# Kernel tuning notes

Measured on AMD Instinct MI355X. Metric: run time of the kernel, lower is better.

The kernel has to match this reference:

```python
import jax, jax.numpy as jnp
import numpy as np

B, S, D, H = 16, 1024, 512, 8
DH = D // H


def setup_inputs() -> dict:
    key = jax.random.key(0)
    ks = jax.random.split(key, 8)
    q = jax.random.normal(ks[0], (B, S, D), dtype=jnp.float32)
    k = jax.random.normal(ks[1], (B, S, D), dtype=jnp.float32)
    v = jax.random.normal(ks[2], (B, S, D), dtype=jnp.float32)
    # causal lower-triangular mask (1 = attend), broadcastable [1,1,S,S]
    mask = jnp.tril(jnp.ones((S, S), dtype=jnp.int32))[None, None]
    # xavier-uniform weights, zero biases (matches _reset_parameters)
    def xavier(rk, fan):
        lim = float(np.sqrt(6.0 / (fan + fan)))
        return jax.random.uniform(rk, (fan, fan), jnp.float32, -lim, lim)
    Wk = xavier(ks[3], D)
    Wv = xavier(ks[4], D)
    Wo = xavier(ks[5], D)
    bk = jnp.zeros((D,), jnp.float32)
    bv = jnp.zeros((D,), jnp.float32)
    bo = jnp.zeros((D,), jnp.float32)
    return {"q": q, "k": k, "v": v, "mask": mask,
            "Wk": Wk, "bk": bk, "Wv": Wv, "bv": bv, "Wo": Wo, "bo": bo,
            "zero_pad": 1}


def reference(q, k, v, mask, Wk, bk, Wv, bv, Wo, bo, zero_pad):
    # key_query_same=True: q and k both use key_linear
    def split_heads(x):  # [B,S,D] -> [B,H,S,DH]
        return x.reshape(B, S, H, DH).transpose(0, 2, 1, 3)

    qh = split_heads(q @ Wk.T + bk)
    kh = split_heads(k @ Wk.T + bk)
    vh = split_heads(v @ Wv.T + bv)

    scores = jnp.einsum('bhqd,bhkd->bhqk', qh, kh) / jnp.sqrt(jnp.float32(DH))
    scores = jnp.where(mask == 0, jnp.float32(-1e32), scores)
    attn = jax.nn.softmax(scores, axis=-1)
    if zero_pad:  # zero out attention of the first query position (simpleKT trick)
        attn = attn.at[:, :, 0, :].set(0.0)
    # dropout p=0.0 (eval) -> identity
    out = jnp.einsum('bhqk,bhkd->bhqd', attn, vh)  # [B,H,S,DH]
    concat = out.transpose(0, 2, 1, 3).reshape(B, S, D)
    return concat @ Wo.T + bo
```

## Files before the change

kernel.cpp:

```cpp
#include <hip/hip_runtime.h>
#include <hip/hip_bf16.h>
#include <math.h>


typedef __attribute__((ext_vector_type(4))) float f32x4;
typedef __attribute__((ext_vector_type(8))) short bf16x8;

__device__ __forceinline__ short f2bf(float f) {
    union { float f; unsigned u; } x; x.f = f;
    unsigned r = x.u + 0x7fffu + ((x.u >> 16) & 1u);
    return (short)(r >> 16);
}
__device__ __forceinline__ short bfscale(short s, float f) {
    union { float f; unsigned u; } x; x.u = ((unsigned)(unsigned short)s) << 16;
    return f2bf(x.f * f);
}
__device__ __forceinline__ unsigned packbf(float a, float b) {
    union { float f; unsigned u; } xa, xb; xa.f = a; xb.f = b;
    return (xa.u >> 16) | (xb.u & 0xffff0000u);
}

__device__ __forceinline__ void gload_lds16(const void* g, void* l) {
    __builtin_amdgcn_global_load_lds(
        (const __attribute__((address_space(1))) unsigned int*)g,
        (__attribute__((address_space(3))) unsigned int*)l, 16, 0, 0);
}

__global__ void cvt_w_kernel(const float* __restrict__ w0, const float* __restrict__ w1,
                             const float* __restrict__ w2,
                             short* __restrict__ o0, short* __restrict__ o1,
                             short* __restrict__ o2)
{
    int z = blockIdx.y;
    const float* src = z == 0 ? w0 : (z == 1 ? w1 : w2);
    short* dst = z == 0 ? o0 : (z == 1 ? o1 : o2);
    int i = (blockIdx.x * 256 + threadIdx.x) * 4;
    float4 f = *(const float4*)(src + i);
    short4 s;
    s.x = f2bf(f.x); s.y = f2bf(f.y); s.z = f2bf(f.z); s.w = f2bf(f.w);
    *(short4*)(dst + i) = s;
}

template<int IN_BF16, int SPLIT>
__device__ __forceinline__ void gemm_body(const void* __restrict__ Xv,
                                          const short* __restrict__ W,
                                          const float* __restrict__ bias,
                                          void* __restrict__ Out,
                                          int m0, int n0)
{
    constexpr int ASTR = IN_BF16 ? 64 : 72;
    __shared__ short As[128 * ASTR];
    __shared__ short Bs[128 * 64];
    int tid = threadIdx.x;
    int lane = tid & 63, w = tid >> 6;
    int wr = (w >> 1) * 64, wc = (w & 1) * 64;
    int fr = lane & 15, hi = lane >> 4;
    int lrow = lane >> 3;
    int gcol = ((lane & 7) ^ (lrow & 3)) * 8;
    int xsw = ((hi ^ (lane & 3)) * 8);
    f32x4 acc[4][4] = {};

    const float* Xf = (const float*)Xv;
    const short* Xb = (const short*)Xv;

    float4 pf[8];
    if (!IN_BF16) {
        #pragma unroll
        for (int p = 0; p < 8; ++p) {
            int e = (p * 256 + tid) * 4;
            pf[p] = *(const float4*)(Xf + (size_t)(m0 + (e >> 6)) * 512 + (e & 63));
        }
    }

    for (int k0 = 0; k0 < 512; k0 += 64) {
        __syncthreads();
        #pragma unroll
        for (int c = 0; c < 4; ++c) {
            int chunk = w * 4 + c;
            gload_lds16(W + (size_t)(n0 + chunk * 8 + lrow) * 512 + k0 + gcol,
                        &Bs[chunk * 512]);
        }
        if (IN_BF16) {
            #pragma unroll
            for (int c = 0; c < 4; ++c) {
                int chunk = w * 4 + c;
                gload_lds16(Xb + (size_t)(m0 + chunk * 8 + lrow) * 512 + k0 + gcol,
                            &As[chunk * 512]);
            }
        } else {
            #pragma unroll
            for (int p = 0; p < 8; ++p) {
                int e = (p * 256 + tid) * 4;
                short4 s;
                s.x = f2bf(pf[p].x); s.y = f2bf(pf[p].y);
                s.z = f2bf(pf[p].z); s.w = f2bf(pf[p].w);
                *(short4*)&As[(e >> 6) * ASTR + (e & 63)] = s;
            }
        }
        __syncthreads();
        if (!IN_BF16 && k0 + 64 < 512) {
            #pragma unroll
            for (int p = 0; p < 8; ++p) {
                int e = (p * 256 + tid) * 4;
                pf[p] = *(const float4*)(Xf + (size_t)(m0 + (e >> 6)) * 512 + k0 + 64 + (e & 63));
            }
        }
        #pragma unroll
        for (int ks = 0; ks < 2; ++ks) {
            bf16x8 a[4], b[4];
            #pragma unroll
            for (int i = 0; i < 4; ++i) {
                int row = wr + i * 16 + fr;
                a[i] = IN_BF16
                    ? *(const bf16x8*)&As[row * ASTR + ks * 32 + xsw]
                    : *(const bf16x8*)&As[row * ASTR + ks * 32 + hi * 8];
            }
            #pragma unroll
            for (int j = 0; j < 4; ++j)
                b[j] = *(const bf16x8*)&Bs[(wc + j * 16 + fr) * 64 + ks * 32 + xsw];
            #pragma unroll
            for (int i = 0; i < 4; ++i)
                #pragma unroll
                for (int j = 0; j < 4; ++j)
                    acc[i][j] = __builtin_amdgcn_mfma_f32_16x16x32_bf16(a[i], b[j], acc[i][j], 0, 0, 0);
        }
    }
    int row4 = (lane >> 4) * 4;
    #pragma unroll
    for (int i = 0; i < 4; ++i) {
        #pragma unroll
        for (int j = 0; j < 4; ++j) {
            int gn = n0 + wc + j * 16 + fr;
            float bb = bias[gn];
            #pragma unroll
            for (int r = 0; r < 4; ++r) {
                int gm = m0 + wr + i * 16 + row4 + r;
                float v = acc[i][j][r] + bb;
                if (SPLIT == 1) {
                    int bidx = gm >> 10, s = gm & 1023, hh = gn >> 6, dh = gn & 63;
                    ((short*)Out)[((((size_t)bidx * 8 + hh) * 1024) + s) * 64 + dh] = f2bf(v);
                } else if (SPLIT == 2) {
                    int bidx = gm >> 10, s = gm & 1023, hh = gn >> 6, dh = gn & 63;
                    ((short*)Out)[((((size_t)bidx * 8 + hh) * 64) + dh) * 1024 + s] = f2bf(v);
                } else {
                    ((float*)Out)[(size_t)gm * 512 + gn] = v;
                }
            }
        }
    }
}

__global__ __launch_bounds__(256, 3) void proj_qk_kernel(
    const float* __restrict__ q, const float* __restrict__ k,
    const short* __restrict__ wk, const float* __restrict__ bk,
    short* __restrict__ qh, short* __restrict__ kh)
{
    int d = blockIdx.x;
    int wg = (d & 7) * 128 + (d >> 3);
    int z = wg >> 9;
    int rem = wg & 511;
    gemm_body<0, 1>(z ? (const void*)k : (const void*)q, wk, bk,
                    z ? (void*)kh : (void*)qh,
                    (rem >> 2) * 128, (rem & 3) * 128);
}

__global__ __launch_bounds__(256, 3) void proj_v_kernel(
    const float* __restrict__ v, const short* __restrict__ wv,
    const float* __restrict__ bv, short* __restrict__ vh)
{
    int d = blockIdx.x;
    int wg = (d & 7) * 64 + (d >> 3);
    gemm_body<0, 2>(v, wv, bv, vh, (wg >> 2) * 128, (wg & 3) * 128);
}

__global__ __launch_bounds__(256, 3) void proj_o_kernel(
    const short* __restrict__ ob, const short* __restrict__ wo,
    const float* __restrict__ bo, float* __restrict__ out)
{
    int d = blockIdx.x;
    int wg = (d & 7) * 64 + (d >> 3);
    gemm_body<1, 0>(ob, wo, bo, out, (wg >> 2) * 128, (wg & 3) * 128);
}

__global__ __launch_bounds__(256, 4) void attn_kernel(
    const short* __restrict__ QH, const short* __restrict__ KH,
    const short* __restrict__ VT, short* __restrict__ O,
    const int* __restrict__ zp)
{
    __shared__ short Ks[2][64][68];
    __shared__ short Vt[2][64][68];
    int tid = threadIdx.x, lane = tid & 63, w = tid >> 6;
    int fr = lane & 15, hi = lane >> 4;
    int d = blockIdx.x;
    int bh = (d & 7) * 16 + ((d >> 3) & 15);
    int qtp = d >> 7;
    const size_t basebh = (size_t)bh << 16;
    const short* Kb = KH + basebh;
    const short* Vb = VT + basebh;
    int r0 = tid >> 3, c0 = (tid & 7) * 8;
    int zero = zp[0];
    int b = bh >> 3, h = bh & 7;
    const float csc = 0.125f * 1.44269504f;
    int srcA = fr + 16 * ((2 * hi) & 3);
    int srcB = fr + 16 * ((2 * hi + 1) & 3);
    bool hi2 = hi >= 2;

    for (int which = 0; which < 2; ++which) {
        int qt = which ? 15 - qtp : qtp;
        int qrow0 = qt * 64 + w * 16;

        bf16x8 aQ[2];
        {
            const short* qp = QH + basebh + (size_t)(qrow0 + fr) * 64 + hi * 8;
            bf16x8 q0 = *(const bf16x8*)qp;
            bf16x8 q1 = *(const bf16x8*)(qp + 32);
            #pragma unroll
            for (int j = 0; j < 8; ++j) {
                aQ[0][j] = bfscale(q0[j], csc);
                aQ[1][j] = bfscale(q1[j], csc);
            }
        }

        f32x4 oacc[4] = {};
        float lsum = 0.f;

        bf16x8 kA, kB, vA, vB;
        kA = *(const bf16x8*)(Kb + r0 * 64 + c0);
        kB = *(const bf16x8*)(Kb + (r0 + 32) * 64 + c0);
        vA = *(const bf16x8*)(Vb + (size_t)r0 * 1024 + c0);
        vB = *(const bf16x8*)(Vb + (size_t)(r0 + 32) * 1024 + c0);
        *(bf16x8*)&Ks[0][r0][c0] = kA;
        *(bf16x8*)&Ks[0][r0 + 32][c0] = kB;
        *(bf16x8*)&Vt[0][r0][c0] = vA;
        *(bf16x8*)&Vt[0][r0 + 32][c0] = vB;
        if (qt > 0) {
            const short* kp = Kb + 4096;
            const short* vp = Vb + 64;
            kA = *(const bf16x8*)(kp + r0 * 64 + c0);
            kB = *(const bf16x8*)(kp + (r0 + 32) * 64 + c0);
            vA = *(const bf16x8*)(vp + (size_t)r0 * 1024 + c0);
            vB = *(const bf16x8*)(vp + (size_t)(r0 + 32) * 1024 + c0);
        }
        __syncthreads();

        for (int kt = 0; kt <= qt; ++kt) {
            int cur = kt & 1;
            if (kt < qt) {
                *(bf16x8*)&Ks[cur ^ 1][r0][c0] = kA;
                *(bf16x8*)&Ks[cur ^ 1][r0 + 32][c0] = kB;
                *(bf16x8*)&Vt[cur ^ 1][r0][c0] = vA;
                *(bf16x8*)&Vt[cur ^ 1][r0 + 32][c0] = vB;
                if (kt + 1 < qt) {
                    const short* kp = Kb + (kt + 2) * 4096;
                    const short* vp = Vb + (kt + 2) * 64;
                    kA = *(const bf16x8*)(kp + r0 * 64 + c0);
                    kB = *(const bf16x8*)(kp + (r0 + 32) * 64 + c0);
                    vA = *(const bf16x8*)(vp + (size_t)r0 * 1024 + c0);
                    vB = *(const bf16x8*)(vp + (size_t)(r0 + 32) * 1024 + c0);
                }
            }

            f32x4 sa[4] = {};
            #pragma unroll
            for (int kf = 0; kf < 4; ++kf)
                #pragma unroll
                for (int ks = 0; ks < 2; ++ks) {
                    bf16x8 kb = *(const bf16x8*)&Ks[cur][kf * 16 + fr][ks * 32 + hi * 8];
                    sa[kf] = __builtin_amdgcn_mfma_f32_16x16x32_bf16(kb, aQ[ks], sa[kf], 0, 0, 0);
                }

            unsigned pk[4][2];
            if (kt == qt) {
                int gq = fr + w * 16;
                #pragma unroll
                for (int kf = 0; kf < 4; ++kf) {
                    float t[4];
                    #pragma unroll
                    for (int r = 0; r < 4; ++r) {
                        int gk = kf * 16 + hi * 4 + r;
                        float p = exp2f(sa[kf][r]);
                        if (gk > gq) p = 0.f;
                        t[r] = p;
                    }
                    lsum += (t[0] + t[1]) + (t[2] + t[3]);
                    pk[kf][0] = packbf(t[0], t[1]);
                    pk[kf][1] = packbf(t[2], t[3]);
                }
            } else {
                #pragma unroll
                for (int kf = 0; kf < 4; ++kf) {
                    float t[4];
                    #pragma unroll
                    for (int r = 0; r < 4; ++r) t[r] = exp2f(sa[kf][r]);
                    lsum += (t[0] + t[1]) + (t[2] + t[3]);
                    pk[kf][0] = packbf(t[0], t[1]);
                    pk[kf][1] = packbf(t[2], t[3]);
                }
            }

            bf16x8 pa[2];
            #pragma unroll
            for (int ks = 0; ks < 2; ++ks) {
                unsigned a0 = __shfl((int)pk[2 * ks][0], srcA);
                unsigned a1 = __shfl((int)pk[2 * ks][1], srcA);
                unsigned b0 = __shfl((int)pk[2 * ks + 1][0], srcA);
                unsigned b1 = __shfl((int)pk[2 * ks + 1][1], srcA);
                unsigned c0w = __shfl((int)pk[2 * ks][0], srcB);
                unsigned c1 = __shfl((int)pk[2 * ks][1], srcB);
                unsigned d0 = __shfl((int)pk[2 * ks + 1][0], srcB);
                unsigned d1 = __shfl((int)pk[2 * ks + 1][1], srcB);
                union { unsigned u[4]; bf16x8 v; } pu;
                pu.u[0] = hi2 ? b0 : a0;
                pu.u[1] = hi2 ? b1 : a1;
                pu.u[2] = hi2 ? d0 : c0w;
                pu.u[3] = hi2 ? d1 : c1;
                pa[ks] = pu.v;
            }

            #pragma unroll
            for (int df = 0; df < 4; ++df)
                #pragma unroll
                for (int ks = 0; ks < 2; ++ks) {
                    bf16x8 vb = *(const bf16x8*)&Vt[cur][df * 16 + fr][ks * 32 + hi * 8];
                    oacc[df] = __builtin_amdgcn_mfma_f32_16x16x32_bf16(pa[ks], vb, oacc[df], 0, 0, 0);
                }
            __syncthreads();
        }

        float rs = lsum;
        rs += __shfl_xor(rs, 16);
        rs += __shfl_xor(rs, 32);
        float inv = 1.0f / rs;
        float invr[4];
        #pragma unroll
        for (int r = 0; r < 4; ++r) invr[r] = __shfl(inv, hi * 4 + r);
        #pragma unroll
        for (int df = 0; df < 4; ++df)
            #pragma unroll
            for (int r = 0; r < 4; ++r) {
                int gq = qrow0 + hi * 4 + r;
                float v = oacc[df][r] * invr[r];
                if (zero && gq == 0) v = 0.f;
                O[((size_t)(b * 1024 + gq)) * 512 + h * 64 + df * 16 + fr] = f2bf(v);
            }
    }
}

extern "C" void kernel_launch(void* const* d_in, const int* in_sizes, int n_in,
                              void* d_out, int out_size, void* d_ws, size_t ws_size,
                              hipStream_t stream)
{
    const float* q  = (const float*)d_in[0];
    const float* k  = (const float*)d_in[1];
    const float* v  = (const float*)d_in[2];
    const float* Wk = (const float*)d_in[4];
    const float* bk = (const float*)d_in[5];
    const float* Wv = (const float*)d_in[6];
    const float* bv = (const float*)d_in[7];
    const float* Wo = (const float*)d_in[8];
    const float* bo = (const float*)d_in[9];
    const int*   zp = (const int*)d_in[10];
    float* out = (float*)d_out;

    short* wkb = (short*)d_ws;
    short* wvb = wkb + 262144;
    short* wob = wvb + 262144;
    short* qh  = wob + 262144;
    short* kh  = qh + 8388608;
    short* vh  = kh + 8388608;
    short* ob  = vh + 8388608;

    cvt_w_kernel<<<dim3(256, 3, 1), 256, 0, stream>>>(Wk, Wv, Wo, wkb, wvb, wob);
    proj_qk_kernel<<<dim3(1024, 1, 1), 256, 0, stream>>>(q, k, wkb, bk, qh, kh);
    proj_v_kernel<<<dim3(512, 1, 1), 256, 0, stream>>>(v, wvb, bv, vh);
    attn_kernel<<<dim3(1024, 1, 1), 256, 0, stream>>>(qh, kh, vh, ob, zp);
    proj_o_kernel<<<dim3(512, 1, 1), 256, 0, stream>>>(ob, wob, bo, out);
}
```

Measured before the change: 122.1 us.

## Share K/V tile loads between paired low and high query tiles

The attention block used to handle its two query tiles (qtp and 15-qtp) one after the other, reloading the K/V tiles each time. Now one pass over the K/V tiles of the high tile also feeds the low tile while kt <= qtL, so each K/V tile is loaded into shared memory only once per block. The cost is a second set of accumulators and Q fragments held in registers, which raises register pressure and may hurt occupancy under launch_bounds(256,4). The zero_pad check is applied only to the low tile, which is the only one that can contain row 0.

```diff
diff --git a/kernel.cpp b/kernel.cpp
--- a/kernel.cpp
+++ b/kernel.cpp
@@ -194,6 +194,7 @@
     int d = blockIdx.x;
     int bh = (d & 7) * 16 + ((d >> 3) & 15);
     int qtp = d >> 7;
+    int qtL = qtp, qtH = 15 - qtp;
     const size_t basebh = (size_t)bh << 16;
     const short* Kb = KH + basebh;
     const short* Vb = VT + basebh;
@@ -204,74 +205,77 @@
     int srcA = fr + 16 * ((2 * hi) & 3);
     int srcB = fr + 16 * ((2 * hi + 1) & 3);
     bool hi2 = hi >= 2;
-
-    for (int which = 0; which < 2; ++which) {
-        int qt = which ? 15 - qtp : qtp;
-        int qrow0 = qt * 64 + w * 16;
-
-        bf16x8 aQ[2];
+    int qrowL = qtL * 64 + w * 16;
+    int qrowH = qtH * 64 + w * 16;
+    int gqloc = fr + w * 16;
+
+    bf16x8 aQL[2], aQH[2];
+    {
+        const short* qpL = QH + basebh + (size_t)(qrowL + fr) * 64 + hi * 8;
+        bf16x8 q0 = *(const bf16x8*)qpL;
+        bf16x8 q1 = *(const bf16x8*)(qpL + 32);
+        const short* qpH = QH + basebh + (size_t)(qrowH + fr) * 64 + hi * 8;
+        bf16x8 q2 = *(const bf16x8*)qpH;
+        bf16x8 q3 = *(const bf16x8*)(qpH + 32);
+        #pragma unroll
+        for (int j = 0; j < 8; ++j) {
+            aQL[0][j] = bfscale(q0[j], csc);
+            aQL[1][j] = bfscale(q1[j], csc);
+            aQH[0][j] = bfscale(q2[j], csc);
+            aQH[1][j] = bfscale(q3[j], csc);
+        }
+    }
+
+    f32x4 oaccL[4] = {}, oaccH[4] = {};
+    float lsumL = 0.f, lsumH = 0.f;
+
+    bf16x8 kA, kB, vA, vB;
+    kA = *(const bf16x8*)(Kb + r0 * 64 + c0);
+    kB = *(const bf16x8*)(Kb + (r0 + 32) * 64 + c0);
+    vA = *(const bf16x8*)(Vb + (size_t)r0 * 1024 + c0);
+    vB = *(const bf16x8*)(Vb + (size_t)(r0 + 32) * 1024 + c0);
+    *(bf16x8*)&Ks[0][r0][c0] = kA;
+    *(bf16x8*)&Ks[0][r0 + 32][c0] = kB;
+    *(bf16x8*)&Vt[0][r0][c0] = vA;
+    *(bf16x8*)&Vt[0][r0 + 32][c0] = vB;
+    {
+        const short* kp = Kb + 4096;
+        const short* vp = Vb + 64;
+        kA = *(const bf16x8*)(kp + r0 * 64 + c0);
+        kB = *(const bf16x8*)(kp + (r0 + 32) * 64 + c0);
+        vA = *(const bf16x8*)(vp + (size_t)r0 * 1024 + c0);
+        vB = *(const bf16x8*)(vp + (size_t)(r0 + 32) * 1024 + c0);
+    }
+    __syncthreads();
+
+    for (int kt = 0; kt <= qtH; ++kt) {
+        int cur = kt & 1;
+        if (kt < qtH) {
+            *(bf16x8*)&Ks[cur ^ 1][r0][c0] = kA;
+            *(bf16x8*)&Ks[cur ^ 1][r0 + 32][c0] = kB;
+            *(bf16x8*)&Vt[cur ^ 1][r0][c0] = vA;
+            *(bf16x8*)&Vt[cur ^ 1][r0 + 32][c0] = vB;
+            if (kt + 1 < qtH) {
+                const short* kp = Kb + (kt + 2) * 4096;
+                const short* vp = Vb + (kt + 2) * 64;
+                kA = *(const bf16x8*)(kp + r0 * 64 + c0);
+                kB = *(const bf16x8*)(kp + (r0 + 32) * 64 + c0);
+                vA = *(const bf16x8*)(vp + (size_t)r0 * 1024 + c0);
+                vB = *(const bf16x8*)(vp + (size_t)(r0 + 32) * 1024 + c0);
+            }
+        }
+
         {
-            const short* qp = QH + basebh + (size_t)(qrow0 + fr) * 64 + hi * 8;
-            bf16x8 q0 = *(const bf16x8*)qp;
-            bf16x8 q1 = *(const bf16x8*)(qp + 32);
-            #pragma unroll
-            for (int j = 0; j < 8; ++j) {
-                aQ[0][j] = bfscale(q0[j], csc);
-                aQ[1][j] = bfscale(q1[j], csc);
-            }
-        }
-
-        f32x4 oacc[4] = {};
-        float lsum = 0.f;
-
-        bf16x8 kA, kB, vA, vB;
-        kA = *(const bf16x8*)(Kb + r0 * 64 + c0);
-        kB = *(const bf16x8*)(Kb + (r0 + 32) * 64 + c0);
-        vA = *(const bf16x8*)(Vb + (size_t)r0 * 1024 + c0);
-        vB = *(const bf16x8*)(Vb + (size_t)(r0 + 32) * 1024 + c0);
-        *(bf16x8*)&Ks[0][r0][c0] = kA;
-        *(bf16x8*)&Ks[0][r0 + 32][c0] = kB;
-        *(bf16x8*)&Vt[0][r0][c0] = vA;
-        *(bf16x8*)&Vt[0][r0 + 32][c0] = vB;
-        if (qt > 0) {
-            const short* kp = Kb + 4096;
-            const short* vp = Vb + 64;
-            kA = *(const bf16x8*)(kp + r0 * 64 + c0);
-            kB = *(const bf16x8*)(kp + (r0 + 32) * 64 + c0);
-            vA = *(const bf16x8*)(vp + (size_t)r0 * 1024 + c0);
-            vB = *(const bf16x8*)(vp + (size_t)(r0 + 32) * 1024 + c0);
-        }
-        __syncthreads();
-
-        for (int kt = 0; kt <= qt; ++kt) {
-            int cur = kt & 1;
-            if (kt < qt) {
-                *(bf16x8*)&Ks[cur ^ 1][r0][c0] = kA;
-                *(bf16x8*)&Ks[cur ^ 1][r0 + 32][c0] = kB;
-                *(bf16x8*)&Vt[cur ^ 1][r0][c0] = vA;
-                *(bf16x8*)&Vt[cur ^ 1][r0 + 32][c0] = vB;
-                if (kt + 1 < qt) {
-                    const short* kp = Kb + (kt + 2) * 4096;
-                    const short* vp = Vb + (kt + 2) * 64;
-                    kA = *(const bf16x8*)(kp + r0 * 64 + c0);
-                    kB = *(const bf16x8*)(kp + (r0 + 32) * 64 + c0);
-                    vA = *(const bf16x8*)(vp + (size_t)r0 * 1024 + c0);
-                    vB = *(const bf16x8*)(vp + (size_t)(r0 + 32) * 1024 + c0);
-                }
-            }
-
             f32x4 sa[4] = {};
             #pragma unroll
             for (int kf = 0; kf < 4; ++kf)
                 #pragma unroll
                 for (int ks = 0; ks < 2; ++ks) {
                     bf16x8 kb = *(const bf16x8*)&Ks[cur][kf * 16 + fr][ks * 32 + hi * 8];
-                    sa[kf] = __builtin_amdgcn_mfma_f32_16x16x32_bf16(kb, aQ[ks], sa[kf], 0, 0, 0);
-                }
-
+                    sa[kf] = __builtin_amdgcn_mfma_f32_16x16x32_bf16(kb, aQH[ks], sa[kf], 0, 0, 0);
+                }
             unsigned pk[4][2];
-            if (kt == qt) {
-                int gq = fr + w * 16;
+            if (kt == qtH) {
                 #pragma unroll
                 for (int kf = 0; kf < 4; ++kf) {
                     float t[4];
@@ -279,10 +283,10 @@
                     for (int r = 0; r < 4; ++r) {
                         int gk = kf * 16 + hi * 4 + r;
                         float p = exp2f(sa[kf][r]);
-                        if (gk > gq) p = 0.f;
+                        if (gk > gqloc) p = 0.f;
                         t[r] = p;
                     }
-                    lsum += (t[0] + t[1]) + (t[2] + t[3]);
+                    lsumH += (t[0] + t[1]) + (t[2] + t[3]);
                     pk[kf][0] = packbf(t[0], t[1]);
                     pk[kf][1] = packbf(t[2], t[3]);
                 }
@@ -292,12 +296,11 @@
                     float t[4];
                     #pragma unroll
                     for (int r = 0; r < 4; ++r) t[r] = exp2f(sa[kf][r]);
-                    lsum += (t[0] + t[1]) + (t[2] + t[3]);
+                    lsumH += (t[0] + t[1]) + (t[2] + t[3]);
                     pk[kf][0] = packbf(t[0], t[1]);
                     pk[kf][1] = packbf(t[2], t[3]);
                 }
             }
-
             bf16x8 pa[2];
             #pragma unroll
             for (int ks = 0; ks < 2; ++ks) {
@@ -316,18 +319,82 @@
                 pu.u[3] = hi2 ? d1 : c1;
                 pa[ks] = pu.v;
             }
-
             #pragma unroll
             for (int df = 0; df < 4; ++df)
                 #pragma unroll
                 for (int ks = 0; ks < 2; ++ks) {
                     bf16x8 vb = *(const bf16x8*)&Vt[cur][df * 16 + fr][ks * 32 + hi * 8];
-                    oacc[df] = __builtin_amdgcn_mfma_f32_16x16x32_bf16(pa[ks], vb, oacc[df], 0, 0, 0);
-                }
-            __syncthreads();
-        }
-
-        float rs = lsum;
+                    oaccH[df] = __builtin_amdgcn_mfma_f32_16x16x32_bf16(pa[ks], vb, oaccH[df], 0, 0, 0);
+                }
+        }
+
+        if (kt <= qtL) {
+            f32x4 sa[4] = {};
+            #pragma unroll
+            for (int kf = 0; kf < 4; ++kf)
+                #pragma unroll
+                for (int ks = 0; ks < 2; ++ks) {
+                    bf16x8 kb = *(const bf16x8*)&Ks[cur][kf * 16 + fr][ks * 32 + hi * 8];
+                    sa[kf] = __builtin_amdgcn_mfma_f32_16x16x32_bf16(kb, aQL[ks], sa[kf], 0, 0, 0);
+                }
+            unsigned pk[4][2];
+            if (kt == qtL) {
+                #pragma unroll
+                for (int kf = 0; kf < 4; ++kf) {
+                    float t[4];
+                    #pragma unroll
+                    for (int r = 0; r < 4; ++r) {
+                        int gk = kf * 16 + hi * 4 + r;
+                        float p = exp2f(sa[kf][r]);
+                        if (gk > gqloc) p = 0.f;
+                        t[r] = p;
+                    }
+                    lsumL += (t[0] + t[1]) + (t[2] + t[3]);
+                    pk[kf][0] = packbf(t[0], t[1]);
+                    pk[kf][1] = packbf(t[2], t[3]);
+                }
+            } else {
+                #pragma unroll
+                for (int kf = 0; kf < 4; ++kf) {
+                    float t[4];
+                    #pragma unroll
+                    for (int r = 0; r < 4; ++r) t[r] = exp2f(sa[kf][r]);
+                    lsumL += (t[0] + t[1]) + (t[2] + t[3]);
+                    pk[kf][0] = packbf(t[0], t[1]);
+                    pk[kf][1] = packbf(t[2], t[3]);
+                }
+            }
+            bf16x8 pa[2];
+            #pragma unroll
+            for (int ks = 0; ks < 2; ++ks) {
+                unsigned a0 = __shfl((int)pk[2 * ks][0], srcA);
+                unsigned a1 = __shfl((int)pk[2 * ks][1], srcA);
+                unsigned b0 = __shfl((int)pk[2 * ks + 1][0], srcA);
+                unsigned b1 = __shfl((int)pk[2 * ks + 1][1], srcA);
+                unsigned c0w = __shfl((int)pk[2 * ks][0], srcB);
+                unsigned c1 = __shfl((int)pk[2 * ks][1], srcB);
+                unsigned d0 = __shfl((int)pk[2 * ks + 1][0], srcB);
+                unsigned d1 = __shfl((int)pk[2 * ks + 1][1], srcB);
+                union { unsigned u[4]; bf16x8 v; } pu;
+                pu.u[0] = hi2 ? b0 : a0;
+                pu.u[1] = hi2 ? b1 : a1;
+                pu.u[2] = hi2 ? d0 : c0w;
+                pu.u[3] = hi2 ? d1 : c1;
+                pa[ks] = pu.v;
+            }
+            #pragma unroll
+            for (int df = 0; df < 4; ++df)
+                #pragma unroll
+                for (int ks = 0; ks < 2; ++ks) {
+                    bf16x8 vb = *(const bf16x8*)&Vt[cur][df * 16 + fr][ks * 32 + hi * 8];
+                    oaccL[df] = __builtin_amdgcn_mfma_f32_16x16x32_bf16(pa[ks], vb, oaccL[df], 0, 0, 0);
+                }
+        }
+        __syncthreads();
+    }
+
+    {
+        float rs = lsumL;
         rs += __shfl_xor(rs, 16);
         rs += __shfl_xor(rs, 32);
         float inv = 1.0f / rs;
@@ -338,9 +405,26 @@
         for (int df = 0; df < 4; ++df)
             #pragma unroll
             for (int r = 0; r < 4; ++r) {
-                int gq = qrow0 + hi * 4 + r;
-                float v = oacc[df][r] * invr[r];
+                int gq = qrowL + hi * 4 + r;
+                float v = oaccL[df][r] * invr[r];
                 if (zero && gq == 0) v = 0.f;
+                O[((size_t)(b * 1024 + gq)) * 512 + h * 64 + df * 16 + fr] = f2bf(v);
+            }
+    }
+    {
+        float rs = lsumH;
+        rs += __shfl_xor(rs, 16);
+        rs += __shfl_xor(rs, 32);
+        float inv = 1.0f / rs;
+        float invr[4];
+        #pragma unroll
+        for (int r = 0; r < 4; ++r) invr[r] = __shfl(inv, hi * 4 + r);
+        #pragma unroll
+        for (int df = 0; df < 4; ++df)
+            #pragma unroll
+            for (int r = 0; r < 4; ++r) {
+                int gq = qrowH + hi * 4 + r;
+                float v = oaccH[df][r] * invr[r];
                 O[((size_t)(b * 1024 + gq)) * 512 + h * 64 + df * 16 + fr] = f2bf(v);
             }
     }
```

After: 192.3 us. 1.57x slower.
